# Kernel optimization log

Hardware: AMD Instinct MI355X
Metric: run time of the kernel (lower is better)

## Reference

```python
import jax, jax.numpy as jnp
import numpy as np

NUM_TREES = 100
VOCAB = 100000
DIM = 32            # dim_leaf_emb
ATT = DIM // 2      # att_dim = 16
BS = 1024

# pair indices matching itertools.combinations(range(n), 2)
_ROW, _COL = np.triu_indices(NUM_TREES, k=1)


def setup_inputs() -> dict:
    key = jax.random.key(0)
    ks = jax.random.split(key, 12)
    x = jax.random.randint(ks[0], (BS, NUM_TREES), 0, VOCAB)
    Emb = jax.random.normal(ks[1], (VOCAB, DIM), dtype=jnp.float32) * 0.02
    W = jax.random.normal(ks[2], (DIM, ATT), dtype=jnp.float32) * (1.0 / np.sqrt(DIM))
    b = jnp.zeros((ATT,), dtype=jnp.float32)
    h = jax.random.normal(ks[3], (ATT,), dtype=jnp.float32) * 0.1
    W1 = jax.random.normal(ks[4], (DIM, DIM // 2), dtype=jnp.float32) * (1.0 / np.sqrt(DIM))
    b1 = jnp.zeros((DIM // 2,), dtype=jnp.float32)
    W2 = jax.random.normal(ks[5], (DIM // 2, DIM // 4), dtype=jnp.float32) * (1.0 / np.sqrt(DIM // 2))
    b2 = jnp.zeros((DIM // 4,), dtype=jnp.float32)
    Wf = jax.random.normal(ks[6], (DIM // 4, 1), dtype=jnp.float32) * (1.0 / np.sqrt(DIM // 4))
    bf = jnp.zeros((1,), dtype=jnp.float32)
    return {"x": x, "Emb": Emb, "W": W, "b": b, "h": h,
            "W1": W1, "b1": b1, "W2": W2, "b2": b2, "Wf": Wf, "bf": bf}


def reference(x, Emb, W, b, h, W1, b1, W2, b2, Wf, bf):
    e = Emb[x]                                   # (bs, T, D)
    half_bip = e[:, _ROW] * e[:, _COL]           # (bs, P, D), P = T*(T-1)/2
    s = jax.nn.relu(jnp.einsum('bpd,da->bpa', half_bip, W) + b)  # (bs, P, A)
    att = jax.nn.softmax(jnp.einsum('bpa,a->bp', s, h), axis=-1) # (bs, P)
    pooled = jnp.einsum('bpd,bp->bd', half_bip, att)             # (bs, D)
    o = jax.nn.relu(pooled @ W1 + b1)
    o = jax.nn.relu(o @ W2 + b2)
    return jax.nn.sigmoid(o @ Wf + bf)           # (bs, 1)
```

## Files before the change

kernel.cpp:

```cpp
#include <hip/hip_runtime.h>
#include <math.h>

constexpr int kT = 100;
constexpr int kP = 4950;
constexpr int kD = 32;
constexpr int kA = 16;
constexpr int kESH = 40;
constexpr int kTiles = (kP + 15) / 16;
constexpr int kTblPad = 4960;
constexpr int kNT = 512;

typedef float    float4v __attribute__((ext_vector_type(4)));
typedef __fp16   fp16x2  __attribute__((ext_vector_type(2)));
typedef __fp16   half4   __attribute__((ext_vector_type(4)));
typedef __fp16   half8   __attribute__((ext_vector_type(8)));
typedef _Float16 half8v  __attribute__((ext_vector_type(8)));

__device__ __forceinline__ void pair_decode(int p, int& r, int& c) {
    const float tq = 39601.0f - 8.0f * (float)p;
    r = (int)((199.0f - sqrtf(tq)) * 0.5f);
    if (r < 0) r = 0;
    if (r > 98) r = 98;
    int base = r * 99 - ((r * (r - 1)) >> 1);
    while (base > p) { --r; base = r * 99 - ((r * (r - 1)) >> 1); }
    while (p - base >= (99 - r)) { base += (99 - r); ++r; }
    c = r + 1 + (p - base);
}

__global__ void pair_init(unsigned short* __restrict__ tbl) {
    const int p = blockIdx.x * 256 + threadIdx.x;
    if (p < kTblPad) {
        int r, c;
        pair_decode(p < kP ? p : kP - 1, r, c);
        tbl[p] = (unsigned short)((r << 8) | c);
    }
}

template <bool USE_TBL>
__global__ __launch_bounds__(kNT, 8)
void afm_kernel(const int* __restrict__ x,
                const float* __restrict__ Emb,
                const float* __restrict__ W,
                const float* __restrict__ bb,
                const float* __restrict__ h,
                const float* __restrict__ W1,
                const float* __restrict__ b1,
                const float* __restrict__ W2,
                const float* __restrict__ b2,
                const float* __restrict__ Wf,
                const float* __restrict__ bf,
                const unsigned short* __restrict__ tbl,
                float* __restrict__ out)
{
    __shared__ __align__(16) unsigned char smem[18432];
    __shared__ float red[8];
    __shared__ float sh_pooled[kD];
    __shared__ float sh_o1[kA];
    __shared__ float sh_o2[8];

    __fp16* she = (__fp16*)smem;
    unsigned short* sh_pair = (unsigned short*)(smem + 8000);

    const int tid  = threadIdx.x;
    const int b    = blockIdx.x;
    const int lane = tid & 63;
    const int wv   = tid >> 6;
    const int quad = lane >> 4;
    const int l15  = lane & 15;
    const int k0   = quad * 8;

    const int* xb = x + b * kT;
    for (int i = tid; i < kT * 8; i += kNT) {
        const int row = i >> 3, c4 = i & 7;
        const int v = xb[row];
        const float4 val = ((const float4*)Emb)[v * 8 + c4];
        union { fp16x2 h2[2]; half4 h4; } tmp;
        tmp.h2[0] = __builtin_amdgcn_cvt_pkrtz(val.x, val.y);
        tmp.h2[1] = __builtin_amdgcn_cvt_pkrtz(val.z, val.w);
        *(half4*)(she + row * kESH + c4 * 4) = tmp.h4;
    }
    if (USE_TBL) {
        const uint4* t4 = (const uint4*)tbl;
        for (int i = tid; i < kTblPad / 8; i += kNT)
            ((uint4*)sh_pair)[i] = t4[i];
    } else {
        for (int p = tid; p < kP; p += kNT) {
            int r, c;
            pair_decode(p, r, c);
            sh_pair[p] = (unsigned short)((r << 8) | c);
        }
    }

    union { fp16x2 h2[4]; half8v h8; } wa;
#pragma unroll
    for (int j = 0; j < 4; ++j)
        wa.h2[j] = __builtin_amdgcn_cvt_pkrtz(W[(k0 + 2 * j) * kA + l15],
                                              W[(k0 + 2 * j + 1) * kA + l15]);
    float h_reg[4];
    float4v bfrag;
#pragma unroll
    for (int rg = 0; rg < 4; ++rg) {
        h_reg[rg] = h[quad * 4 + rg];
        bfrag[rg] = bb[quad * 4 + rg];
    }
    __syncthreads();

    float pool[8];
#pragma unroll
    for (int j = 0; j < 8; ++j) pool[j] = 0.0f;
    float lsum = 0.0f;

#pragma unroll 2
    for (int t = wv; t < kTiles; t += 8) {
        const int p_raw = t * 16 + l15;
        const int p = p_raw < kP ? p_raw : kP - 1;
        const unsigned pr = sh_pair[p];
        const int roff = (int)(pr >> 8) * kESH;
        const int coff = (int)(pr & 255) * kESH;

        const half8 er = *(const half8*)(she + roff + k0);
        const half8 ec = *(const half8*)(she + coff + k0);
        union { half8 fp; half8v mf; } hb;
        hb.fp = er * ec;

        float4v acc = __builtin_amdgcn_mfma_f32_16x16x32_f16(wa.h8, hb.mf, bfrag, 0, 0, 0);

        float part = 0.0f;
#pragma unroll
        for (int rg = 0; rg < 4; ++rg)
            part = fmaf(fmaxf(acc[rg], 0.0f), h_reg[rg], part);
        part += __shfl_xor(part, 16, 64);
        part += __shfl_xor(part, 32, 64);

        const float w = (p_raw < kP) ? __expf(part) : 0.0f;
        lsum += w;
#pragma unroll
        for (int j = 0; j < 8; ++j)
            pool[j] = fmaf(w, (float)hb.fp[j], pool[j]);
    }

#pragma unroll
    for (int off = 1; off < 64; off <<= 1) lsum += __shfl_xor(lsum, off, 64);
    if (lane == 0) red[wv] = lsum;

    __syncthreads();
    float* stg = (float*)smem;
#pragma unroll
    for (int j = 0; j < 8; ++j) stg[tid * 9 + j] = pool[j];
    __syncthreads();

    if (tid < kD) {
        const float invS = 4.0f / (red[0] + red[1] + red[2] + red[3] +
                                   red[4] + red[5] + red[6] + red[7]);
        const int q = tid >> 3, j = tid & 7;
        float s = 0.0f;
        for (int w8 = 0; w8 < 8; ++w8)
            for (int l = 0; l < 16; ++l)
                s += stg[(w8 * 64 + q * 16 + l) * 9 + j];
        sh_pooled[tid] = s * invS;
    }
    __syncthreads();

    if (tid < kA) {
        float o = b1[tid];
#pragma unroll
        for (int d = 0; d < kD; ++d) o = fmaf(sh_pooled[d], W1[d * kA + tid], o);
        sh_o1[tid] = fmaxf(o, 0.0f);
    }
    __syncthreads();
    if (tid < 8) {
        float o = b2[tid];
#pragma unroll
        for (int a = 0; a < kA; ++a) o = fmaf(sh_o1[a], W2[a * 8 + tid], o);
        sh_o2[tid] = fmaxf(o, 0.0f);
    }
    __syncthreads();
    if (tid == 0) {
        float z = bf[0];
#pragma unroll
        for (int j = 0; j < 8; ++j) z = fmaf(sh_o2[j], Wf[j], z);
        out[b] = 1.0f / (1.0f + __expf(-z));
    }
}

extern "C" void kernel_launch(void* const* d_in, const int* in_sizes, int n_in,
                              void* d_out, int out_size, void* d_ws, size_t ws_size,
                              hipStream_t stream) {
    const int*   x   = (const int*)d_in[0];
    const float* Emb = (const float*)d_in[1];
    const float* W   = (const float*)d_in[2];
    const float* bb  = (const float*)d_in[3];
    const float* h   = (const float*)d_in[4];
    const float* W1  = (const float*)d_in[5];
    const float* b1  = (const float*)d_in[6];
    const float* W2  = (const float*)d_in[7];
    const float* b2  = (const float*)d_in[8];
    const float* Wf  = (const float*)d_in[9];
    const float* bf  = (const float*)d_in[10];
    float* out = (float*)d_out;

    if (ws_size >= (size_t)(kTblPad * 2)) {
        unsigned short* tbl = (unsigned short*)d_ws;
        pair_init<<<(kTblPad + 255) / 256, 256, 0, stream>>>(tbl);
        afm_kernel<true><<<1024, kNT, 0, stream>>>(x, Emb, W, bb, h, W1, b1, W2, b2,
                                                   Wf, bf, tbl, out);
    } else {
        afm_kernel<false><<<1024, kNT, 0, stream>>>(x, Emb, W, bb, h, W1, b1, W2, b2,
                                                    Wf, bf, nullptr, out);
    }
}
```

Measured before the change: 113.7 us.

## Factor pair scores as (W∘e_r)·e_c block tiles and drop pair table

```diff
diff --git a/kernel.cpp b/kernel.cpp
--- a/kernel.cpp
+++ b/kernel.cpp
@@ -2,13 +2,11 @@
 #include <math.h>
 
 constexpr int kT = 100;
-constexpr int kP = 4950;
 constexpr int kD = 32;
 constexpr int kA = 16;
 constexpr int kESH = 40;
-constexpr int kTiles = (kP + 15) / 16;
-constexpr int kTblPad = 4960;
-constexpr int kNT = 512;
+constexpr int kNT = 448;
+constexpr int kNW = 7;
 
 typedef float    float4v __attribute__((ext_vector_type(4)));
 typedef __fp16   fp16x2  __attribute__((ext_vector_type(2)));
@@ -16,28 +14,17 @@
 typedef __fp16   half8   __attribute__((ext_vector_type(8)));
 typedef _Float16 half8v  __attribute__((ext_vector_type(8)));
 
-__device__ __forceinline__ void pair_decode(int p, int& r, int& c) {
-    const float tq = 39601.0f - 8.0f * (float)p;
-    r = (int)((199.0f - sqrtf(tq)) * 0.5f);
-    if (r < 0) r = 0;
-    if (r > 98) r = 98;
-    int base = r * 99 - ((r * (r - 1)) >> 1);
-    while (base > p) { --r; base = r * 99 - ((r * (r - 1)) >> 1); }
-    while (p - base >= (99 - r)) { base += (99 - r); ++r; }
-    c = r + 1 + (p - base);
-}
-
-__global__ void pair_init(unsigned short* __restrict__ tbl) {
-    const int p = blockIdx.x * 256 + threadIdx.x;
-    if (p < kTblPad) {
-        int r, c;
-        pair_decode(p < kP ? p : kP - 1, r, c);
-        tbl[p] = (unsigned short)((r << 8) | c);
-    }
-}
-
-template <bool USE_TBL>
-__global__ __launch_bounds__(kNT, 8)
+__device__ __constant__ unsigned int kUnits[28] = {
+    0u|(0u<<8)|(15u<<16),  16u|(16u<<8)|(15u<<16), 0u|(16u<<8)|(16u<<16),  0u|(32u<<8)|(16u<<16),
+    32u|(32u<<8)|(15u<<16),48u|(48u<<8)|(15u<<16), 0u|(48u<<8)|(16u<<16),  0u|(64u<<8)|(16u<<16),
+    64u|(64u<<8)|(15u<<16),80u|(80u<<8)|(15u<<16), 0u|(80u<<8)|(16u<<16),  0u|(96u<<8)|(16u<<16),
+    16u|(32u<<8)|(16u<<16),16u|(48u<<8)|(16u<<16),16u|(64u<<8)|(16u<<16), 16u|(80u<<8)|(16u<<16),
+    16u|(96u<<8)|(16u<<16),32u|(48u<<8)|(16u<<16),32u|(64u<<8)|(16u<<16), 32u|(80u<<8)|(16u<<16),
+    32u|(96u<<8)|(16u<<16),48u|(64u<<8)|(16u<<16),48u|(80u<<8)|(16u<<16), 48u|(96u<<8)|(16u<<16),
+    64u|(80u<<8)|(16u<<16),64u|(96u<<8)|(16u<<16),80u|(96u<<8)|(16u<<16), 96u|(96u<<8)|(3u<<16)
+};
+
+__global__ __launch_bounds__(kNT, 7)
 void afm_kernel(const int* __restrict__ x,
                 const float* __restrict__ Emb,
                 const float* __restrict__ W,
@@ -49,17 +36,15 @@
                 const float* __restrict__ b2,
                 const float* __restrict__ Wf,
                 const float* __restrict__ bf,
-                const unsigned short* __restrict__ tbl,
                 float* __restrict__ out)
 {
-    __shared__ __align__(16) unsigned char smem[18432];
-    __shared__ float red[8];
+    __shared__ __align__(16) unsigned char smem[16128];
+    __shared__ float red[kNW];
     __shared__ float sh_pooled[kD];
     __shared__ float sh_o1[kA];
     __shared__ float sh_o2[8];
 
     __fp16* she = (__fp16*)smem;
-    unsigned short* sh_pair = (unsigned short*)(smem + 8000);
 
     const int tid  = threadIdx.x;
     const int b    = blockIdx.x;
@@ -79,19 +64,8 @@
         tmp.h2[1] = __builtin_amdgcn_cvt_pkrtz(val.z, val.w);
         *(half4*)(she + row * kESH + c4 * 4) = tmp.h4;
     }
-    if (USE_TBL) {
-        const uint4* t4 = (const uint4*)tbl;
-        for (int i = tid; i < kTblPad / 8; i += kNT)
-            ((uint4*)sh_pair)[i] = t4[i];
-    } else {
-        for (int p = tid; p < kP; p += kNT) {
-            int r, c;
-            pair_decode(p, r, c);
-            sh_pair[p] = (unsigned short)((r << 8) | c);
-        }
-    }
-
-    union { fp16x2 h2[4]; half8v h8; } wa;
+
+    union { fp16x2 h2[4]; half8 fp; } wa;
 #pragma unroll
     for (int j = 0; j < 4; ++j)
         wa.h2[j] = __builtin_amdgcn_cvt_pkrtz(W[(k0 + 2 * j) * kA + l15],
@@ -108,40 +82,68 @@
     float pool[8];
 #pragma unroll
     for (int j = 0; j < 8; ++j) pool[j] = 0.0f;
-    float lsum = 0.0f;
-
-#pragma unroll 2
-    for (int t = wv; t < kTiles; t += 8) {
-        const int p_raw = t * 16 + l15;
-        const int p = p_raw < kP ? p_raw : kP - 1;
-        const unsigned pr = sh_pair[p];
-        const int roff = (int)(pr >> 8) * kESH;
-        const int coff = (int)(pr & 255) * kESH;
-
-        const half8 er = *(const half8*)(she + roff + k0);
-        const half8 ec = *(const half8*)(she + coff + k0);
-        union { half8 fp; half8v mf; } hb;
-        hb.fp = er * ec;
-
-        float4v acc = __builtin_amdgcn_mfma_f32_16x16x32_f16(wa.h8, hb.mf, bfrag, 0, 0, 0);
-
-        float part = 0.0f;
-#pragma unroll
-        for (int rg = 0; rg < 4; ++rg)
-            part = fmaf(fmaxf(acc[rg], 0.0f), h_reg[rg], part);
-        part += __shfl_xor(part, 16, 64);
-        part += __shfl_xor(part, 32, 64);
-
-        const float w = (p_raw < kP) ? __expf(part) : 0.0f;
-        lsum += w;
+    float wsum = 0.0f;
+
+    for (int u = 0; u < 4; ++u) {
+        const unsigned ud = kUnits[wv * 4 + u];
+        const int R  = ud & 255;
+        const int C  = (ud >> 8) & 255;
+        const int nr = ud >> 16;
+        const int c  = C + l15;
+        const int cl = c < 100 ? c : 99;
+
+        union { half8 fp; half8v mf; } ec;
+        ec.fp = *(const half8*)(she + cl * kESH + k0);
+
+        float accu[8];
+#pragma unroll
+        for (int j = 0; j < 8; ++j) accu[j] = 0.0f;
+
+        for (int rr = 0; rr < nr; rr += 2) {
+            const int r1 = R + rr, r2 = R + rr + 1;
+            const half8 er1 = *(const half8*)(she + r1 * kESH + k0);
+            const half8 er2 = *(const half8*)(she + r2 * kESH + k0);
+            union { half8 fp; half8v mf; } a1, a2;
+            a1.fp = wa.fp * er1;
+            a2.fp = wa.fp * er2;
+
+            float4v s1 = __builtin_amdgcn_mfma_f32_16x16x32_f16(a1.mf, ec.mf, bfrag, 0, 0, 0);
+            float4v s2 = __builtin_amdgcn_mfma_f32_16x16x32_f16(a2.mf, ec.mf, bfrag, 0, 0, 0);
+
+            float p1 = 0.0f, p2 = 0.0f;
+#pragma unroll
+            for (int rg = 0; rg < 4; ++rg) {
+                p1 = fmaf(fmaxf(s1[rg], 0.0f), h_reg[rg], p1);
+                p2 = fmaf(fmaxf(s2[rg], 0.0f), h_reg[rg], p2);
+            }
+            union { fp16x2 hh; int ii; } t0, t1;
+            t0.hh = __builtin_amdgcn_cvt_pkrtz(p1, p2);
+            t1.ii = __shfl_xor(t0.ii, 16, 64);
+            t0.hh = t0.hh + t1.hh;
+            t1.ii = __shfl_xor(t0.ii, 32, 64);
+            t0.hh = t0.hh + t1.hh;
+            const float l1 = (float)t0.hh[0];
+            const float l2 = (float)t0.hh[1];
+
+            const bool v1 = (c > r1) && (c < 100);
+            const bool v2 = (rr + 1 < nr) && (c > r2) && (c < 100);
+            const float w1 = v1 ? __expf(l1) : 0.0f;
+            const float w2 = v2 ? __expf(l2) : 0.0f;
+            wsum += w1 + w2;
+#pragma unroll
+            for (int j = 0; j < 8; ++j) {
+                accu[j] = fmaf(w1, (float)er1[j], accu[j]);
+                accu[j] = fmaf(w2, (float)er2[j], accu[j]);
+            }
+        }
 #pragma unroll
         for (int j = 0; j < 8; ++j)
-            pool[j] = fmaf(w, (float)hb.fp[j], pool[j]);
-    }
-
-#pragma unroll
-    for (int off = 1; off < 64; off <<= 1) lsum += __shfl_xor(lsum, off, 64);
-    if (lane == 0) red[wv] = lsum;
+            pool[j] = fmaf((float)ec.fp[j], accu[j], pool[j]);
+    }
+
+#pragma unroll
+    for (int off = 1; off < 64; off <<= 1) wsum += __shfl_xor(wsum, off, 64);
+    if (lane == 0) red[wv] = wsum;
 
     __syncthreads();
     float* stg = (float*)smem;
@@ -150,13 +152,14 @@
     __syncthreads();
 
     if (tid < kD) {
-        const float invS = 4.0f / (red[0] + red[1] + red[2] + red[3] +
-                                   red[4] + red[5] + red[6] + red[7]);
+        float ls = 0.0f;
+        for (int w7 = 0; w7 < kNW; ++w7) ls += red[w7];
+        const float invS = 4.0f / ls;
         const int q = tid >> 3, j = tid & 7;
         float s = 0.0f;
-        for (int w8 = 0; w8 < 8; ++w8)
+        for (int w7 = 0; w7 < kNW; ++w7)
             for (int l = 0; l < 16; ++l)
-                s += stg[(w8 * 64 + q * 16 + l) * 9 + j];
+                s += stg[(w7 * 64 + q * 16 + l) * 9 + j];
         sh_pooled[tid] = s * invS;
     }
     __syncthreads();
@@ -199,13 +202,5 @@
     const float* bf  = (const float*)d_in[10];
     float* out = (float*)d_out;
 
-    if (ws_size >= (size_t)(kTblPad * 2)) {
-        unsigned short* tbl = (unsigned short*)d_ws;
-        pair_init<<<(kTblPad + 255) / 256, 256, 0, stream>>>(tbl);
-        afm_kernel<true><<<1024, kNT, 0, stream>>>(x, Emb, W, bb, h, W1, b1, W2, b2,
-                                                   Wf, bf, tbl, out);
-    } else {
-        afm_kernel<false><<<1024, kNT, 0, stream>>>(x, Emb, W, bb, h, W1, b1, W2, b2,
-                                                    Wf, bf, nullptr, out);
-    }
+    afm_kernel<<<1024, kNT, 0, stream>>>(x, Emb, W, bb, h, W1, b1, W2, b2, Wf, bf, out);
 }
```

Measured after the change: 127.7 us. +12.3%, slower.
